# Performance work log

Measured on AMD Instinct MI355X. Metric: run time of the kernel, lower is better.

Reference implementation:

```python
import jax, jax.numpy as jnp
import numpy as np

N = 50000          # nodes
E = 1_600_000      # edges (avg degree 32)
FEAT = 128         # nfeat == nhid
HID = 128
L = 3              # nconvs
C = 10             # nclass
G = 128            # graphs in batch
BN_EPS = 1e-5


def setup_inputs() -> dict:
    key = jax.random.key(0)
    ks = jax.random.split(key, 8)
    x = jax.random.normal(ks[0], (N, FEAT), dtype=jnp.float32)
    edge_index = jax.random.randint(ks[1], (2, E), 0, N, dtype=jnp.int64)
    batch = jnp.sort(jax.random.randint(ks[2], (N,), 0, G, dtype=jnp.int64))
    # stacked per-layer MLP params (nfeat == nhid so shapes are uniform)
    W1 = jax.random.normal(ks[3], (L, FEAT, HID), dtype=jnp.float32) * 0.05
    b1 = jnp.zeros((L, HID), dtype=jnp.float32)
    W2 = jax.random.normal(ks[4], (L, HID, HID), dtype=jnp.float32) * 0.05
    b2 = jnp.zeros((L, HID), dtype=jnp.float32)
    # BatchNorm (eval mode: running stats)
    gamma = jnp.ones((L, HID), dtype=jnp.float32)
    beta = jnp.zeros((L, HID), dtype=jnp.float32)
    rmean = jnp.zeros((L, HID), dtype=jnp.float32)
    rvar = jnp.ones((L, HID), dtype=jnp.float32)
    fc_w = jax.random.normal(ks[5], (HID, C), dtype=jnp.float32) * 0.05
    fc_b = jnp.zeros((C,), dtype=jnp.float32)
    return {
        "x": x, "edge_index": edge_index, "batch": batch,
        "W1": W1, "b1": b1, "W2": W2, "b2": b2,
        "gamma": gamma, "beta": beta, "rmean": rmean, "rvar": rvar,
        "fc_w": fc_w, "fc_b": fc_b,
    }


def reference(x, edge_index, batch, W1, b1, W2, b2, gamma, beta, rmean, rvar, fc_w, fc_b):
    src, dst = edge_index[0], edge_index[1]
    for l in range(L):
        # GINConv aggregation: h_i = (1 + eps) * x_i + sum_{j -> i} x_j  (eps = 0)
        agg = jax.ops.segment_sum(x[src], dst, num_segments=N)  # [N, d] scatter-add
        h = x + agg
        # MLP: Linear -> ReLU -> Linear -> BatchNorm (eval: running stats)
        h = jax.nn.relu(h @ W1[l] + b1[l])
        h = h @ W2[l] + b2[l]
        h = (h - rmean[l]) * jax.lax.rsqrt(rvar[l] + BN_EPS) * gamma[l] + beta[l]
        # outer ReLU; dropout is identity at inference
        x = jax.nn.relu(h)
    # global mean pool over batch ids
    counts = jax.ops.segment_sum(jnp.ones((N,), x.dtype), batch, num_segments=G)
    pooled = jax.ops.segment_sum(x, batch, num_segments=G)
    pooled = pooled / jnp.clip(counts, 1.0)[:, None]  # [G, HID]
    logits = pooled @ fc_w + fc_b                      # [G, C]
    return jax.nn.log_softmax(logits, axis=1)
```

## Files before the change

kernel.cpp:

```cpp
#include <hip/hip_runtime.h>

#define NN 50000
#define EE 1600000
#define GG 128
#define NC 10

#define SB_N   49
#define SB_PAD 36864
#define BK_N   782
#define BK_PAD 2560
#define CHUNK  4096
#define NBLK1  391
#define SLICES 9

typedef __attribute__((ext_vector_type(8))) short bf16x8;
typedef __attribute__((ext_vector_type(4))) float f32x4;
typedef unsigned short u16;

__device__ inline u16 f2bf(float x){
  unsigned u = __builtin_bit_cast(unsigned, x);
  u += 0x7fffu + ((u >> 16) & 1u);
  return (u16)(u >> 16);
}
__device__ inline float bf2f(u16 u){
  return __builtin_bit_cast(float, ((unsigned)u) << 16);
}

__global__ void k_zero_int(int* __restrict__ p, int n){
  int i = blockIdx.x * 256 + threadIdx.x;
  if (i < n) p[i] = 0;
}

__global__ __launch_bounds__(256) void k_scatL1(const int* __restrict__ srcI, const int* __restrict__ dstI,
                                                int* __restrict__ scur, int* __restrict__ sstg){
  __shared__ int hist[SB_N];
  __shared__ int base[64];
  __shared__ int gadj[SB_N];
  __shared__ unsigned reo[CHUNK];
  int t = threadIdx.x;
  int e0 = blockIdx.x * CHUNK;
  int cnt = EE - e0; if (cnt > CHUNK) cnt = CHUNK;
  if (t < SB_N) hist[t] = 0;
  __syncthreads();
  unsigned p[16]; int rk[16];
  #pragma unroll
  for (int r = 0; r < 16; ++r){
    int i = r * 256 + t;
    if (i < cnt){
      unsigned d = (unsigned)dstI[e0 + i];
      p[r] = (d << 16) | (unsigned)srcI[e0 + i];
      rk[r] = atomicAdd(&hist[d >> 10], 1);
    }
  }
  __syncthreads();
  if (t < 64) base[t] = (t < SB_N) ? hist[t] : 0;
  __syncthreads();
  for (int off = 1; off < 64; off <<= 1){
    int a = (t < 64 && t >= off) ? base[t - off] : 0;
    __syncthreads();
    if (t < 64) base[t] += a;
    __syncthreads();
  }
  if (t < SB_N){
    int ex = base[t] - hist[t];
    gadj[t] = atomicAdd(&scur[t], hist[t]) - ex;
  }
  __syncthreads();
  #pragma unroll
  for (int r = 0; r < 16; ++r){
    int i = r * 256 + t;
    if (i < cnt){
      unsigned sb = p[r] >> 26;
      reo[(base[sb] - hist[sb]) + rk[r]] = p[r];
    }
  }
  __syncthreads();
  for (int q = t; q < cnt; q += 256){
    unsigned v = reo[q];
    unsigned sb = v >> 26;
    int off = gadj[sb] + q;
    if ((unsigned)off < SB_PAD) sstg[sb * SB_PAD + off] = (int)v;
  }
}

__global__ __launch_bounds__(256) void k_scatL2(const int* __restrict__ sstg, const int* __restrict__ scur,
                                                int* __restrict__ bcur, int* __restrict__ bstg){
  __shared__ int hist[16];
  __shared__ int base[16];
  __shared__ int gadj[16];
  __shared__ unsigned reo[CHUNK];
  int t = threadIdx.x;
  int sb = blockIdx.x / SLICES;
  int sl = blockIdx.x % SLICES;
  int ssz = scur[sb]; if (ssz > SB_PAD) ssz = SB_PAD;
  int i0 = sl * CHUNK;
  int cnt = ssz - i0;
  if (cnt <= 0) return;
  if (cnt > CHUNK) cnt = CHUNK;
  if (t < 16) hist[t] = 0;
  __syncthreads();
  unsigned p[16]; int rk[16];
  #pragma unroll
  for (int r = 0; r < 16; ++r){
    int i = r * 256 + t;
    if (i < cnt){
      p[r] = (unsigned)sstg[sb * SB_PAD + i0 + i];
      rk[r] = atomicAdd(&hist[(p[r] >> 22) & 15], 1);
    }
  }
  __syncthreads();
  if (t < 16) base[t] = hist[t];
  __syncthreads();
  for (int off = 1; off < 16; off <<= 1){
    int a = (t < 16 && t >= off) ? base[t - off] : 0;
    __syncthreads();
    if (t < 16) base[t] += a;
    __syncthreads();
  }
  if (t < 16){
    int ex = base[t] - hist[t];
    gadj[t] = atomicAdd(&bcur[sb * 16 + t], hist[t]) - ex;
  }
  __syncthreads();
  #pragma unroll
  for (int r = 0; r < 16; ++r){
    int i = r * 256 + t;
    if (i < cnt){
      unsigned b = (p[r] >> 22) & 15;
      reo[(base[b] - hist[b]) + rk[r]] = p[r];
    }
  }
  __syncthreads();
  for (int q = t; q < cnt; q += 256){
    unsigned v = reo[q];
    unsigned b = (v >> 22) & 15;
    int off = gadj[b] + q;
    if ((unsigned)off < BK_PAD) bstg[(sb * 16 + b) * BK_PAD + off] = (int)v;
  }
}

__global__ __launch_bounds__(256) void k_finalize(const int* __restrict__ bstg, const int* __restrict__ bcur,
                                                  u16* __restrict__ adj, int2* __restrict__ ndinfo){
  __shared__ unsigned ebuf[BK_PAD];
  __shared__ int hist[64];
  __shared__ int lrs[64];
  __shared__ int lcur[64];
  int b = blockIdx.x;
  int t = threadIdx.x;
  int bsz = bcur[b]; if (bsz > BK_PAD) bsz = BK_PAD;
  if (t < 64) hist[t] = 0;
  __syncthreads();
  for (int i = t; i < bsz; i += 256){
    unsigned p = (unsigned)bstg[b * BK_PAD + i];
    ebuf[i] = p;
    atomicAdd(&hist[(p >> 16) & 63], 1);
  }
  __syncthreads();
  if (t < 64) lrs[t] = hist[t];
  __syncthreads();
  for (int off = 1; off < 64; off <<= 1){
    int a = (t < 64 && t >= off) ? lrs[t - off] : 0;
    __syncthreads();
    if (t < 64) lrs[t] += a;
    __syncthreads();
  }
  if (t < 64){
    int ex = lrs[t] - hist[t];
    lcur[t] = ex;
    int node = b * 64 + t;
    if (node < NN) ndinfo[node] = make_int2(b * BK_PAD + ex, hist[t]);
  }
  __syncthreads();
  for (int i = t; i < bsz; i += 256){
    unsigned p = ebuf[i];
    int slot = atomicAdd(&lcur[(p >> 16) & 63], 1);
    adj[b * BK_PAD + slot] = (u16)(p & 0xffffu);
  }
}

__global__ void k_prep(const float* __restrict__ x, const float* __restrict__ W1f, const float* __restrict__ W2f,
                       const float* __restrict__ b1, const float* __restrict__ b2,
                       const float* __restrict__ gma, const float* __restrict__ bta,
                       const float* __restrict__ rmn, const float* __restrict__ rvr,
                       u16* __restrict__ xb, u16* __restrict__ Wt,
                       float* __restrict__ SC, float* __restrict__ SH){
  int bid = blockIdx.x;
  int t = threadIdx.x;
  if (bid < 6250){
    int i = bid * 256 + t;
    float4 v = ((const float4*)x)[i];
    ushort4 o;
    o.x = f2bf(v.x); o.y = f2bf(v.y); o.z = f2bf(v.z); o.w = f2bf(v.w);
    ((ushort4*)xb)[i] = o;
  } else if (bid < 6634){
    int i = (bid - 6250) * 256 + t;
    int a = i >> 14; int r = i & 16383; int n = r >> 7; int k = r & 127;
    const float* Wsrc = (a < 3) ? (W1f + a * 16384) : (W2f + (a - 3) * 16384);
    Wt[a * 16384 + n * 128 + k] = f2bf(Wsrc[k * 128 + n]);
  } else {
    for (int i = t; i < 768; i += 256){
      int l = i >> 8; int r = i & 255; int mode = r >> 7; int c = r & 127;
      if (mode == 0){
        SC[(l * 2) * 128 + c] = 1.0f;
        SH[(l * 2) * 128 + c] = b1[l * 128 + c];
      } else {
        float S = gma[l * 128 + c] * rsqrtf(rvr[l * 128 + c] + 1e-5f);
        SC[(l * 2 + 1) * 128 + c] = S;
        SH[(l * 2 + 1) * 128 + c] = (b2[l * 128 + c] - rmn[l * 128 + c]) * S + bta[l * 128 + c];
      }
    }
  }
}

__global__ __launch_bounds__(256) void k_agg(const u16* __restrict__ xb, u16* __restrict__ hb,
                                             const u16* __restrict__ adj,
                                             const int2* __restrict__ ndinfo){
  int t = threadIdx.x;
  int node = blockIdx.x * 16 + (t >> 4);
  int lane = t & 15;
  const bf16x8* xv = (const bf16x8*)xb;
  bf16x8 sv = xv[(long)node * 16 + lane];
  float a[8];
  #pragma unroll
  for (int j = 0; j < 8; ++j) a[j] = bf2f((u16)sv[j]);
  int2 nd = ndinfo[node];
  int r0 = nd.x;
  int d  = nd.y;
  int j = 0;
  for (; j + 8 <= d; j += 8){
    bf16x8 v[8];
    #pragma unroll
    for (int u = 0; u < 8; ++u){
      int s = adj[r0 + j + u];
      v[u] = xv[(long)s * 16 + lane];
    }
    #pragma unroll
    for (int q = 0; q < 8; ++q){
      float s01 = bf2f((u16)v[0][q]) + bf2f((u16)v[1][q]);
      float s23 = bf2f((u16)v[2][q]) + bf2f((u16)v[3][q]);
      float s45 = bf2f((u16)v[4][q]) + bf2f((u16)v[5][q]);
      float s67 = bf2f((u16)v[6][q]) + bf2f((u16)v[7][q]);
      a[q] += (s01 + s23) + (s45 + s67);
    }
  }
  for (; j + 4 <= d; j += 4){
    bf16x8 v0 = xv[(long)adj[r0 + j + 0] * 16 + lane];
    bf16x8 v1 = xv[(long)adj[r0 + j + 1] * 16 + lane];
    bf16x8 v2 = xv[(long)adj[r0 + j + 2] * 16 + lane];
    bf16x8 v3 = xv[(long)adj[r0 + j + 3] * 16 + lane];
    #pragma unroll
    for (int q = 0; q < 8; ++q)
      a[q] += (bf2f((u16)v0[q]) + bf2f((u16)v1[q])) + (bf2f((u16)v2[q]) + bf2f((u16)v3[q]));
  }
  for (; j < d; ++j){
    bf16x8 v0 = xv[(long)adj[r0 + j] * 16 + lane];
    #pragma unroll
    for (int q = 0; q < 8; ++q) a[q] += bf2f((u16)v0[q]);
  }
  bf16x8 o;
  #pragma unroll
  for (int j2 = 0; j2 < 8; ++j2) o[j2] = (short)f2bf(a[j2]);
  ((bf16x8*)hb)[(long)node * 16 + lane] = o;
}

template<int POOL>
__global__ __launch_bounds__(256, 2) void k_mlp(const u16* __restrict__ Ain,
                                                const u16* __restrict__ Wt1,
                                                const u16* __restrict__ Wt2,
                                                const float* __restrict__ B1,
                                                const float* __restrict__ SC2,
                                                const float* __restrict__ SH2,
                                                const int* __restrict__ batch,
                                                u16* __restrict__ Out,
                                                float* __restrict__ pooled){
  __shared__ u16 W2s[16384];
  __shared__ u16 Hs[4][16][128];
  __shared__ float P1[128], P2[128], P3[128];
  int t = threadIdx.x;

  #pragma unroll
  for (int i = 0; i < 8; ++i){
    int c = t + 256 * i;
    int r = c >> 4, cc = c & 15;
    unsigned byte = (unsigned)(r * 256 + cc * 16) ^ (unsigned)((r & 7) << 4);
    *(bf16x8*)((char*)W2s + byte) = *(const bf16x8*)(Wt2 + c * 8);
  }
  if (t < 128){ P1[t] = B1[t]; P2[t] = SC2[t]; P3[t] = SH2[t]; }

  int wv = t >> 6;
  int l  = t & 63;
  int m  = l & 15;
  int kb = l >> 4;

  bf16x8 w1[8][4];
  #pragma unroll
  for (int mt = 0; mt < 8; ++mt)
    #pragma unroll
    for (int ks = 0; ks < 4; ++ks)
      w1[mt][ks] = *(const bf16x8*)(Wt1 + (mt * 16 + m) * 128 + ks * 32 + kb * 8);

  __syncthreads();

  char* hs = (char*)&Hs[wv][0][0];
  unsigned mswz = (unsigned)((m & 7) << 4);
  int gw = blockIdx.x * 4 + wv;
  const int NW = gridDim.x * 4;

  for (int tile = gw; tile < 3125; tile += NW){
    long row0 = (long)tile * 16;
    f32x4 acc[8] = {};
    #pragma unroll
    for (int ks = 0; ks < 4; ++ks){
      bf16x8 h = *(const bf16x8*)(Ain + (row0 + m) * 128 + ks * 32 + kb * 8);
      #pragma unroll
      for (int mt = 0; mt < 8; ++mt)
        acc[mt] = __builtin_amdgcn_mfma_f32_16x16x32_bf16(w1[mt][ks], h, acc[mt], 0, 0, 0);
    }
    #pragma unroll
    for (int mt = 0; mt < 8; ++mt){
      int c0 = mt * 16 + kb * 4;
      float4 bb = *(const float4*)&P1[c0];
      ushort4 o;
      o.x = f2bf(fmaxf(acc[mt][0] + bb.x, 0.f));
      o.y = f2bf(fmaxf(acc[mt][1] + bb.y, 0.f));
      o.z = f2bf(fmaxf(acc[mt][2] + bb.z, 0.f));
      o.w = f2bf(fmaxf(acc[mt][3] + bb.w, 0.f));
      unsigned byte = (unsigned)(m * 256 + c0 * 2) ^ mswz;
      *(ushort4*)(hs + byte) = o;
    }
    f32x4 acc2[8] = {};
    #pragma unroll
    for (int ks = 0; ks < 4; ++ks){
      unsigned hb_ = (unsigned)(m * 256 + ks * 64 + kb * 16) ^ mswz;
      bf16x8 h2 = *(const bf16x8*)(hs + hb_);
      #pragma unroll
      for (int mt = 0; mt < 8; ++mt){
        unsigned wb = (unsigned)((mt * 16 + m) * 256 + ks * 64 + kb * 16) ^ mswz;
        bf16x8 w2 = *(const bf16x8*)((char*)W2s + wb);
        acc2[mt] = __builtin_amdgcn_mfma_f32_16x16x32_bf16(w2, h2, acc2[mt], 0, 0, 0);
      }
    }
    if (!POOL){
      #pragma unroll
      for (int mt = 0; mt < 8; ++mt){
        int c0 = mt * 16 + kb * 4;
        float4 sc = *(const float4*)&P2[c0];
        float4 sh = *(const float4*)&P3[c0];
        ushort4 o;
        o.x = f2bf(fmaxf(acc2[mt][0] * sc.x + sh.x, 0.f));
        o.y = f2bf(fmaxf(acc2[mt][1] * sc.y + sh.y, 0.f));
        o.z = f2bf(fmaxf(acc2[mt][2] * sc.z + sh.z, 0.f));
        o.w = f2bf(fmaxf(acc2[mt][3] * sc.w + sh.w, 0.f));
        *(ushort4*)(Out + (row0 + m) * 128 + c0) = o;
      }
    } else {
      int b0 = batch[row0];
      int b15 = batch[row0 + 15];
      if (b0 == b15){
        #pragma unroll
        for (int mt = 0; mt < 8; ++mt){
          int c0 = mt * 16 + kb * 4;
          float4 sc = *(const float4*)&P2[c0];
          float4 sh = *(const float4*)&P3[c0];
          float v0 = fmaxf(acc2[mt][0] * sc.x + sh.x, 0.f);
          float v1 = fmaxf(acc2[mt][1] * sc.y + sh.y, 0.f);
          float v2 = fmaxf(acc2[mt][2] * sc.z + sh.z, 0.f);
          float v3 = fmaxf(acc2[mt][3] * sc.w + sh.w, 0.f);
          #pragma unroll
          for (int off = 1; off < 16; off <<= 1){
            v0 += __shfl_xor(v0, off);
            v1 += __shfl_xor(v1, off);
            v2 += __shfl_xor(v2, off);
            v3 += __shfl_xor(v3, off);
          }
          if (m == 0){
            float* pg = pooled + b0 * 128 + c0;
            atomicAdd(pg + 0, v0); atomicAdd(pg + 1, v1);
            atomicAdd(pg + 2, v2); atomicAdd(pg + 3, v3);
          }
        }
      } else {
        int bm = batch[row0 + m];
        #pragma unroll
        for (int mt = 0; mt < 8; ++mt){
          int c0 = mt * 16 + kb * 4;
          float4 sc = *(const float4*)&P2[c0];
          float4 sh = *(const float4*)&P3[c0];
          float* pg = pooled + bm * 128 + c0;
          atomicAdd(pg + 0, fmaxf(acc2[mt][0] * sc.x + sh.x, 0.f));
          atomicAdd(pg + 1, fmaxf(acc2[mt][1] * sc.y + sh.y, 0.f));
          atomicAdd(pg + 2, fmaxf(acc2[mt][2] * sc.z + sh.z, 0.f));
          atomicAdd(pg + 3, fmaxf(acc2[mt][3] * sc.w + sh.w, 0.f));
        }
      }
    }
  }
}

__global__ void k_head(const float* __restrict__ pooled, const float* __restrict__ fcw,
                       const float* __restrict__ fcb, const int* __restrict__ batch,
                       float* __restrict__ out){
  int g = threadIdx.x;
  int lo, hi;
  { int a = 0, b = NN; while (a < b){ int mm = (a + b) >> 1; if (batch[mm] < g) a = mm + 1; else b = mm; } lo = a; }
  { int a = lo, b = NN; while (a < b){ int mm = (a + b) >> 1; if (batch[mm] < g + 1) a = mm + 1; else b = mm; } hi = a; }
  float inv = 1.0f / fmaxf((float)(hi - lo), 1.0f);
  float logit[NC];
  #pragma unroll
  for (int c = 0; c < NC; ++c) logit[c] = fcb[c];
  for (int k = 0; k < 128; ++k){
    float pv = pooled[g * 128 + k] * inv;
    #pragma unroll
    for (int c = 0; c < NC; ++c) logit[c] += pv * fcw[k * NC + c];
  }
  float m = logit[0];
  #pragma unroll
  for (int c = 1; c < NC; ++c) m = fmaxf(m, logit[c]);
  float sum = 0.f;
  #pragma unroll
  for (int c = 0; c < NC; ++c) sum += expf(logit[c] - m);
  float ls = logf(sum);
  #pragma unroll
  for (int c = 0; c < NC; ++c) out[g * NC + c] = logit[c] - m - ls;
}

extern "C" void kernel_launch(void* const* d_in, const int* in_sizes, int n_in,
                              void* d_out, int out_size, void* d_ws, size_t ws_size,
                              hipStream_t stream) {
  const float* x     = (const float*)d_in[0];
  const int*   eidx  = (const int*)  d_in[1];
  const int*   batch = (const int*)  d_in[2];
  const float* W1    = (const float*)d_in[3];
  const float* b1    = (const float*)d_in[4];
  const float* W2    = (const float*)d_in[5];
  const float* b2    = (const float*)d_in[6];
  const float* gma   = (const float*)d_in[7];
  const float* bta   = (const float*)d_in[8];
  const float* rmn   = (const float*)d_in[9];
  const float* rvr   = (const float*)d_in[10];
  const float* fcw   = (const float*)d_in[11];
  const float* fcb   = (const float*)d_in[12];
  float* out = (float*)d_out;

  const int* srcI = eidx;
  const int* dstI = eidx + EE;

  u16* bufX = (u16*)d_ws;
  u16* bufA = bufX + 6400000;
  u16* bufB = bufA + 6400000;
  u16* Wt   = bufB + 6400000;
  float* SC = (float*)(Wt + 98304);
  float* SH = SC + 768;
  float* pooled = SH + 768;
  int* ctr  = (int*)(pooled + 16384);
  int* scur = ctr;
  int* bcur = ctr + 64;
  u16* adj  = (u16*)(ctr + 848);
  int2* ndinfo = (int2*)(adj + (BK_N * BK_PAD));
  int* sstg = (int*)bufA;
  int* bstg = (int*)bufB;

  k_zero_int<<<68, 256, 0, stream>>>((int*)pooled, 16384 + 848);

  k_scatL1  <<<NBLK1, 256, 0, stream>>>(srcI, dstI, scur, sstg);
  k_scatL2  <<<SB_N * SLICES, 256, 0, stream>>>(sstg, scur, bcur, bstg);
  k_finalize<<<BK_N, 256, 0, stream>>>(bstg, bcur, adj, ndinfo);

  k_prep<<<6635, 256, 0, stream>>>(x, W1, W2, b1, b2, gma, bta, rmn, rvr, bufX, Wt, SC, SH);

  k_agg   <<<3125, 256, 0, stream>>>(bufX, bufA, adj, ndinfo);
  k_mlp<0><<<391, 256, 0, stream>>>(bufA, Wt + 0 * 16384, Wt + 3 * 16384,
                                    SH + 0 * 128, SC + 1 * 128, SH + 1 * 128, batch, bufB, pooled);
  k_agg   <<<3125, 256, 0, stream>>>(bufB, bufA, adj, ndinfo);
  k_mlp<0><<<391, 256, 0, stream>>>(bufA, Wt + 1 * 16384, Wt + 4 * 16384,
                                    SH + 2 * 128, SC + 3 * 128, SH + 3 * 128, batch, bufB, pooled);
  k_agg   <<<3125, 256, 0, stream>>>(bufB, bufA, adj, ndinfo);
  k_mlp<1><<<391, 256, 0, stream>>>(bufA, Wt + 2 * 16384, Wt + 5 * 16384,
                                    SH + 4 * 128, SC + 5 * 128, SH + 5 * 128, batch, bufB, pooled);

  k_head<<<1, 128, 0, stream>>>(pooled, fcw, fcb, batch, out);
}
```

Measured before the change: 473.0 us.

## Split MLP output columns across waves, keep both weight slices in registers

The fused MLP kernel now has the four waves of a block share one 16-row tile, with each wave computing 32 of the 128 output columns. The first layer's output goes through double-buffered shared memory with a block barrier. Both W1 and W2 slices live in registers, which removes the 32KB shared W2 copy and its per-tile LDS reads, and the grid grows from 391 to 1024 blocks with a higher occupancy hint. In exchange it adds a __syncthreads per tile, each wave re-reads the same input rows, and each wave issues fewer MFMAs per load.

```diff
diff --git a/kernel.cpp b/kernel.cpp
--- a/kernel.cpp
+++ b/kernel.cpp
@@ -264,7 +264,7 @@
 }
 
 template<int POOL>
-__global__ __launch_bounds__(256, 2) void k_mlp(const u16* __restrict__ Ain,
+__global__ __launch_bounds__(256, 4) void k_mlp(const u16* __restrict__ Ain,
                                                 const u16* __restrict__ Wt1,
                                                 const u16* __restrict__ Wt2,
                                                 const float* __restrict__ B1,
@@ -273,84 +273,71 @@
                                                 const int* __restrict__ batch,
                                                 u16* __restrict__ Out,
                                                 float* __restrict__ pooled){
-  __shared__ u16 W2s[16384];
-  __shared__ u16 Hs[4][16][128];
+  __shared__ u16 Hs[2][16][128];
   __shared__ float P1[128], P2[128], P3[128];
   int t = threadIdx.x;
-
-  #pragma unroll
-  for (int i = 0; i < 8; ++i){
-    int c = t + 256 * i;
-    int r = c >> 4, cc = c & 15;
-    unsigned byte = (unsigned)(r * 256 + cc * 16) ^ (unsigned)((r & 7) << 4);
-    *(bf16x8*)((char*)W2s + byte) = *(const bf16x8*)(Wt2 + c * 8);
-  }
   if (t < 128){ P1[t] = B1[t]; P2[t] = SC2[t]; P3[t] = SH2[t]; }
 
   int wv = t >> 6;
   int l  = t & 63;
   int m  = l & 15;
   int kb = l >> 4;
-
-  bf16x8 w1[8][4];
-  #pragma unroll
-  for (int mt = 0; mt < 8; ++mt)
-    #pragma unroll
-    for (int ks = 0; ks < 4; ++ks)
-      w1[mt][ks] = *(const bf16x8*)(Wt1 + (mt * 16 + m) * 128 + ks * 32 + kb * 8);
-
-  __syncthreads();
-
-  char* hs = (char*)&Hs[wv][0][0];
+  int mt0 = wv * 2;
+
+  bf16x8 w1[2][4], w2[2][4];
+  #pragma unroll
+  for (int mtl = 0; mtl < 2; ++mtl)
+    #pragma unroll
+    for (int ks = 0; ks < 4; ++ks){
+      w1[mtl][ks] = *(const bf16x8*)(Wt1 + ((mt0 + mtl) * 16 + m) * 128 + ks * 32 + kb * 8);
+      w2[mtl][ks] = *(const bf16x8*)(Wt2 + ((mt0 + mtl) * 16 + m) * 128 + ks * 32 + kb * 8);
+    }
+  __syncthreads();
+
   unsigned mswz = (unsigned)((m & 7) << 4);
-  int gw = blockIdx.x * 4 + wv;
-  const int NW = gridDim.x * 4;
-
-  for (int tile = gw; tile < 3125; tile += NW){
+
+  for (int tile = blockIdx.x; tile < 3125; tile += gridDim.x){
     long row0 = (long)tile * 16;
-    f32x4 acc[8] = {};
+    char* hs = (char*)&Hs[tile & 1][0][0];
+    f32x4 acc0 = {}, acc1 = {};
     #pragma unroll
     for (int ks = 0; ks < 4; ++ks){
       bf16x8 h = *(const bf16x8*)(Ain + (row0 + m) * 128 + ks * 32 + kb * 8);
-      #pragma unroll
-      for (int mt = 0; mt < 8; ++mt)
-        acc[mt] = __builtin_amdgcn_mfma_f32_16x16x32_bf16(w1[mt][ks], h, acc[mt], 0, 0, 0);
-    }
-    #pragma unroll
-    for (int mt = 0; mt < 8; ++mt){
-      int c0 = mt * 16 + kb * 4;
+      acc0 = __builtin_amdgcn_mfma_f32_16x16x32_bf16(w1[0][ks], h, acc0, 0, 0, 0);
+      acc1 = __builtin_amdgcn_mfma_f32_16x16x32_bf16(w1[1][ks], h, acc1, 0, 0, 0);
+    }
+    #pragma unroll
+    for (int mtl = 0; mtl < 2; ++mtl){
+      const f32x4& av = mtl ? acc1 : acc0;
+      int c0 = (mt0 + mtl) * 16 + kb * 4;
       float4 bb = *(const float4*)&P1[c0];
       ushort4 o;
-      o.x = f2bf(fmaxf(acc[mt][0] + bb.x, 0.f));
-      o.y = f2bf(fmaxf(acc[mt][1] + bb.y, 0.f));
-      o.z = f2bf(fmaxf(acc[mt][2] + bb.z, 0.f));
-      o.w = f2bf(fmaxf(acc[mt][3] + bb.w, 0.f));
-      unsigned byte = (unsigned)(m * 256 + c0 * 2) ^ mswz;
-      *(ushort4*)(hs + byte) = o;
-    }
-    f32x4 acc2[8] = {};
+      o.x = f2bf(fmaxf(av[0] + bb.x, 0.f));
+      o.y = f2bf(fmaxf(av[1] + bb.y, 0.f));
+      o.z = f2bf(fmaxf(av[2] + bb.z, 0.f));
+      o.w = f2bf(fmaxf(av[3] + bb.w, 0.f));
+      *(ushort4*)(hs + ((unsigned)(m * 256 + c0 * 2) ^ mswz)) = o;
+    }
+    __syncthreads();
+    f32x4 acc2_0 = {}, acc2_1 = {};
     #pragma unroll
     for (int ks = 0; ks < 4; ++ks){
-      unsigned hb_ = (unsigned)(m * 256 + ks * 64 + kb * 16) ^ mswz;
-      bf16x8 h2 = *(const bf16x8*)(hs + hb_);
-      #pragma unroll
-      for (int mt = 0; mt < 8; ++mt){
-        unsigned wb = (unsigned)((mt * 16 + m) * 256 + ks * 64 + kb * 16) ^ mswz;
-        bf16x8 w2 = *(const bf16x8*)((char*)W2s + wb);
-        acc2[mt] = __builtin_amdgcn_mfma_f32_16x16x32_bf16(w2, h2, acc2[mt], 0, 0, 0);
-      }
+      bf16x8 h2 = *(const bf16x8*)(hs + ((unsigned)(m * 256 + ks * 64 + kb * 16) ^ mswz));
+      acc2_0 = __builtin_amdgcn_mfma_f32_16x16x32_bf16(w2[0][ks], h2, acc2_0, 0, 0, 0);
+      acc2_1 = __builtin_amdgcn_mfma_f32_16x16x32_bf16(w2[1][ks], h2, acc2_1, 0, 0, 0);
     }
     if (!POOL){
       #pragma unroll
-      for (int mt = 0; mt < 8; ++mt){
-        int c0 = mt * 16 + kb * 4;
+      for (int mtl = 0; mtl < 2; ++mtl){
+        const f32x4& av = mtl ? acc2_1 : acc2_0;
+        int c0 = (mt0 + mtl) * 16 + kb * 4;
         float4 sc = *(const float4*)&P2[c0];
         float4 sh = *(const float4*)&P3[c0];
         ushort4 o;
-        o.x = f2bf(fmaxf(acc2[mt][0] * sc.x + sh.x, 0.f));
-        o.y = f2bf(fmaxf(acc2[mt][1] * sc.y + sh.y, 0.f));
-        o.z = f2bf(fmaxf(acc2[mt][2] * sc.z + sh.z, 0.f));
-        o.w = f2bf(fmaxf(acc2[mt][3] * sc.w + sh.w, 0.f));
+        o.x = f2bf(fmaxf(av[0] * sc.x + sh.x, 0.f));
+        o.y = f2bf(fmaxf(av[1] * sc.y + sh.y, 0.f));
+        o.z = f2bf(fmaxf(av[2] * sc.z + sh.z, 0.f));
+        o.w = f2bf(fmaxf(av[3] * sc.w + sh.w, 0.f));
         *(ushort4*)(Out + (row0 + m) * 128 + c0) = o;
       }
     } else {
@@ -358,14 +345,15 @@
       int b15 = batch[row0 + 15];
       if (b0 == b15){
         #pragma unroll
-        for (int mt = 0; mt < 8; ++mt){
-          int c0 = mt * 16 + kb * 4;
+        for (int mtl = 0; mtl < 2; ++mtl){
+          const f32x4& av = mtl ? acc2_1 : acc2_0;
+          int c0 = (mt0 + mtl) * 16 + kb * 4;
           float4 sc = *(const float4*)&P2[c0];
           float4 sh = *(const float4*)&P3[c0];
-          float v0 = fmaxf(acc2[mt][0] * sc.x + sh.x, 0.f);
-          float v1 = fmaxf(acc2[mt][1] * sc.y + sh.y, 0.f);
-          float v2 = fmaxf(acc2[mt][2] * sc.z + sh.z, 0.f);
-          float v3 = fmaxf(acc2[mt][3] * sc.w + sh.w, 0.f);
+          float v0 = fmaxf(av[0] * sc.x + sh.x, 0.f);
+          float v1 = fmaxf(av[1] * sc.y + sh.y, 0.f);
+          float v2 = fmaxf(av[2] * sc.z + sh.z, 0.f);
+          float v3 = fmaxf(av[3] * sc.w + sh.w, 0.f);
           #pragma unroll
           for (int off = 1; off < 16; off <<= 1){
             v0 += __shfl_xor(v0, off);
@@ -382,15 +370,16 @@
       } else {
         int bm = batch[row0 + m];
         #pragma unroll
-        for (int mt = 0; mt < 8; ++mt){
-          int c0 = mt * 16 + kb * 4;
+        for (int mtl = 0; mtl < 2; ++mtl){
+          const f32x4& av = mtl ? acc2_1 : acc2_0;
+          int c0 = (mt0 + mtl) * 16 + kb * 4;
           float4 sc = *(const float4*)&P2[c0];
           float4 sh = *(const float4*)&P3[c0];
           float* pg = pooled + bm * 128 + c0;
-          atomicAdd(pg + 0, fmaxf(acc2[mt][0] * sc.x + sh.x, 0.f));
-          atomicAdd(pg + 1, fmaxf(acc2[mt][1] * sc.y + sh.y, 0.f));
-          atomicAdd(pg + 2, fmaxf(acc2[mt][2] * sc.z + sh.z, 0.f));
-          atomicAdd(pg + 3, fmaxf(acc2[mt][3] * sc.w + sh.w, 0.f));
+          atomicAdd(pg + 0, fmaxf(av[0] * sc.x + sh.x, 0.f));
+          atomicAdd(pg + 1, fmaxf(av[1] * sc.y + sh.y, 0.f));
+          atomicAdd(pg + 2, fmaxf(av[2] * sc.z + sh.z, 0.f));
+          atomicAdd(pg + 3, fmaxf(av[3] * sc.w + sh.w, 0.f));
         }
       }
     }
@@ -469,14 +458,14 @@
   k_prep<<<6635, 256, 0, stream>>>(x, W1, W2, b1, b2, gma, bta, rmn, rvr, bufX, Wt, SC, SH);
 
   k_agg   <<<3125, 256, 0, stream>>>(bufX, bufA, adj, ndinfo);
-  k_mlp<0><<<391, 256, 0, stream>>>(bufA, Wt + 0 * 16384, Wt + 3 * 16384,
-                                    SH + 0 * 128, SC + 1 * 128, SH + 1 * 128, batch, bufB, pooled);
+  k_mlp<0><<<1024, 256, 0, stream>>>(bufA, Wt + 0 * 16384, Wt + 3 * 16384,
+                                     SH + 0 * 128, SC + 1 * 128, SH + 1 * 128, batch, bufB, pooled);
   k_agg   <<<3125, 256, 0, stream>>>(bufB, bufA, adj, ndinfo);
-  k_mlp<0><<<391, 256, 0, stream>>>(bufA, Wt + 1 * 16384, Wt + 4 * 16384,
-                                    SH + 2 * 128, SC + 3 * 128, SH + 3 * 128, batch, bufB, pooled);
+  k_mlp<0><<<1024, 256, 0, stream>>>(bufA, Wt + 1 * 16384, Wt + 4 * 16384,
+                                     SH + 2 * 128, SC + 3 * 128, SH + 3 * 128, batch, bufB, pooled);
   k_agg   <<<3125, 256, 0, stream>>>(bufB, bufA, adj, ndinfo);
-  k_mlp<1><<<391, 256, 0, stream>>>(bufA, Wt + 2 * 16384, Wt + 5 * 16384,
-                                    SH + 4 * 128, SC + 5 * 128, SH + 5 * 128, batch, bufB, pooled);
+  k_mlp<1><<<1024, 256, 0, stream>>>(bufA, Wt + 2 * 16384, Wt + 5 * 16384,
+                                     SH + 4 * 128, SC + 5 * 128, SH + 5 * 128, batch, bufB, pooled);
 
   k_head<<<1, 128, 0, stream>>>(pooled, fcw, fcb, batch, out);
 }
```

Result: faster. 400.3 us (-15.4%).

## Stage both MLP weight matrices in LDS and prefetch next tile's activations

Applied to the files above, without the earlier changes.

The first-layer weights move out of the per-thread register array (128 VGPRs of fragments) into swizzled shared memory alongside W2. This frees registers, and the freed space is used to software-prefetch the next tile's input rows while the current tile's second GEMM and epilogue run. Bias and BN scale/shift are now read straight from global memory instead of LDS, and the grid grows from 391 to 512 blocks. The trade is more LDS traffic (64KB of weights per block, which may limit occupancy) in exchange for lower register pressure and better overlap of memory latency.

```diff
diff --git a/kernel.cpp b/kernel.cpp
--- a/kernel.cpp
+++ b/kernel.cpp
@@ -273,79 +273,90 @@
                                                 const int* __restrict__ batch,
                                                 u16* __restrict__ Out,
                                                 float* __restrict__ pooled){
-  __shared__ u16 W2s[16384];
-  __shared__ u16 Hs[4][16][128];
-  __shared__ float P1[128], P2[128], P3[128];
-  int t = threadIdx.x;
-
-  #pragma unroll
-  for (int i = 0; i < 8; ++i){
-    int c = t + 256 * i;
-    int r = c >> 4, cc = c & 15;
-    unsigned byte = (unsigned)(r * 256 + cc * 16) ^ (unsigned)((r & 7) << 4);
-    *(bf16x8*)((char*)W2s + byte) = *(const bf16x8*)(Wt2 + c * 8);
-  }
-  if (t < 128){ P1[t] = B1[t]; P2[t] = SC2[t]; P3[t] = SH2[t]; }
+  __shared__ u16 Wl[2][16384];
+  __shared__ u16 Hb[4][2048];
+  int t = threadIdx.x;
+
+  #pragma unroll
+  for (int w = 0; w < 2; ++w){
+    const u16* src = w ? Wt2 : Wt1;
+    #pragma unroll
+    for (int i = 0; i < 8; ++i){
+      int c = t + 256 * i;
+      int r = c >> 4, cc = c & 15;
+      unsigned byte = (unsigned)(r * 256 + cc * 16) ^ (unsigned)((r & 7) << 4);
+      *(bf16x8*)((char*)Wl[w] + byte) = *(const bf16x8*)(src + c * 8);
+    }
+  }
+  __syncthreads();
 
   int wv = t >> 6;
   int l  = t & 63;
   int m  = l & 15;
   int kb = l >> 4;
-
-  bf16x8 w1[8][4];
-  #pragma unroll
-  for (int mt = 0; mt < 8; ++mt)
-    #pragma unroll
-    for (int ks = 0; ks < 4; ++ks)
-      w1[mt][ks] = *(const bf16x8*)(Wt1 + (mt * 16 + m) * 128 + ks * 32 + kb * 8);
-
-  __syncthreads();
-
-  char* hs = (char*)&Hs[wv][0][0];
+  char* hb  = (char*)Hb[wv];
+  char* w1p = (char*)Wl[0];
+  char* w2p = (char*)Wl[1];
   unsigned mswz = (unsigned)((m & 7) << 4);
-  int gw = blockIdx.x * 4 + wv;
+
+  int tile = blockIdx.x * 4 + wv;
   const int NW = gridDim.x * 4;
-
-  for (int tile = gw; tile < 3125; tile += NW){
+  bf16x8 h[4];
+  if (tile < 3125){
+    long r = (long)tile * 16 + m;
+    #pragma unroll
+    for (int ks = 0; ks < 4; ++ks) h[ks] = *(const bf16x8*)(Ain + r * 128 + ks * 32 + kb * 8);
+  }
+
+  while (tile < 3125){
     long row0 = (long)tile * 16;
     f32x4 acc[8] = {};
     #pragma unroll
-    for (int ks = 0; ks < 4; ++ks){
-      bf16x8 h = *(const bf16x8*)(Ain + (row0 + m) * 128 + ks * 32 + kb * 8);
+    for (int mt = 0; mt < 8; ++mt){
+      unsigned rb = (unsigned)((mt * 16 + m) * 256) ^ mswz;
       #pragma unroll
-      for (int mt = 0; mt < 8; ++mt)
-        acc[mt] = __builtin_amdgcn_mfma_f32_16x16x32_bf16(w1[mt][ks], h, acc[mt], 0, 0, 0);
+      for (int ks = 0; ks < 4; ++ks){
+        bf16x8 wf = *(const bf16x8*)(w1p + (rb ^ (unsigned)(ks * 64 + kb * 16)));
+        acc[mt] = __builtin_amdgcn_mfma_f32_16x16x32_bf16(wf, h[ks], acc[mt], 0, 0, 0);
+      }
+    }
+    int ntile = tile + NW;
+    if (ntile < 3125){
+      long r = (long)ntile * 16 + m;
+      #pragma unroll
+      for (int ks = 0; ks < 4; ++ks) h[ks] = *(const bf16x8*)(Ain + r * 128 + ks * 32 + kb * 8);
     }
     #pragma unroll
     for (int mt = 0; mt < 8; ++mt){
       int c0 = mt * 16 + kb * 4;
-      float4 bb = *(const float4*)&P1[c0];
+      float4 bb = *(const float4*)(B1 + c0);
       ushort4 o;
       o.x = f2bf(fmaxf(acc[mt][0] + bb.x, 0.f));
       o.y = f2bf(fmaxf(acc[mt][1] + bb.y, 0.f));
       o.z = f2bf(fmaxf(acc[mt][2] + bb.z, 0.f));
       o.w = f2bf(fmaxf(acc[mt][3] + bb.w, 0.f));
-      unsigned byte = (unsigned)(m * 256 + c0 * 2) ^ mswz;
-      *(ushort4*)(hs + byte) = o;
-    }
+      *(ushort4*)(hb + ((unsigned)(m * 256 + c0 * 2) ^ mswz)) = o;
+    }
+    bf16x8 h2[4];
+    #pragma unroll
+    for (int ks = 0; ks < 4; ++ks)
+      h2[ks] = *(const bf16x8*)(hb + ((unsigned)(m * 256 + ks * 64 + kb * 16) ^ mswz));
     f32x4 acc2[8] = {};
     #pragma unroll
-    for (int ks = 0; ks < 4; ++ks){
-      unsigned hb_ = (unsigned)(m * 256 + ks * 64 + kb * 16) ^ mswz;
-      bf16x8 h2 = *(const bf16x8*)(hs + hb_);
+    for (int mt = 0; mt < 8; ++mt){
+      unsigned rb = (unsigned)((mt * 16 + m) * 256) ^ mswz;
       #pragma unroll
-      for (int mt = 0; mt < 8; ++mt){
-        unsigned wb = (unsigned)((mt * 16 + m) * 256 + ks * 64 + kb * 16) ^ mswz;
-        bf16x8 w2 = *(const bf16x8*)((char*)W2s + wb);
-        acc2[mt] = __builtin_amdgcn_mfma_f32_16x16x32_bf16(w2, h2, acc2[mt], 0, 0, 0);
+      for (int ks = 0; ks < 4; ++ks){
+        bf16x8 wf = *(const bf16x8*)(w2p + (rb ^ (unsigned)(ks * 64 + kb * 16)));
+        acc2[mt] = __builtin_amdgcn_mfma_f32_16x16x32_bf16(wf, h2[ks], acc2[mt], 0, 0, 0);
       }
     }
     if (!POOL){
       #pragma unroll
       for (int mt = 0; mt < 8; ++mt){
         int c0 = mt * 16 + kb * 4;
-        float4 sc = *(const float4*)&P2[c0];
-        float4 sh = *(const float4*)&P3[c0];
+        float4 sc = *(const float4*)(SC2 + c0);
+        float4 sh = *(const float4*)(SH2 + c0);
         ushort4 o;
         o.x = f2bf(fmaxf(acc2[mt][0] * sc.x + sh.x, 0.f));
         o.y = f2bf(fmaxf(acc2[mt][1] * sc.y + sh.y, 0.f));
@@ -360,8 +371,8 @@
         #pragma unroll
         for (int mt = 0; mt < 8; ++mt){
           int c0 = mt * 16 + kb * 4;
-          float4 sc = *(const float4*)&P2[c0];
-          float4 sh = *(const float4*)&P3[c0];
+          float4 sc = *(const float4*)(SC2 + c0);
+          float4 sh = *(const float4*)(SH2 + c0);
           float v0 = fmaxf(acc2[mt][0] * sc.x + sh.x, 0.f);
           float v1 = fmaxf(acc2[mt][1] * sc.y + sh.y, 0.f);
           float v2 = fmaxf(acc2[mt][2] * sc.z + sh.z, 0.f);
@@ -384,8 +395,8 @@
         #pragma unroll
         for (int mt = 0; mt < 8; ++mt){
           int c0 = mt * 16 + kb * 4;
-          float4 sc = *(const float4*)&P2[c0];
-          float4 sh = *(const float4*)&P3[c0];
+          float4 sc = *(const float4*)(SC2 + c0);
+          float4 sh = *(const float4*)(SH2 + c0);
           float* pg = pooled + bm * 128 + c0;
           atomicAdd(pg + 0, fmaxf(acc2[mt][0] * sc.x + sh.x, 0.f));
           atomicAdd(pg + 1, fmaxf(acc2[mt][1] * sc.y + sh.y, 0.f));
@@ -394,6 +405,7 @@
         }
       }
     }
+    tile = ntile;
   }
 }
 
@@ -469,13 +481,13 @@
   k_prep<<<6635, 256, 0, stream>>>(x, W1, W2, b1, b2, gma, bta, rmn, rvr, bufX, Wt, SC, SH);
 
   k_agg   <<<3125, 256, 0, stream>>>(bufX, bufA, adj, ndinfo);
-  k_mlp<0><<<391, 256, 0, stream>>>(bufA, Wt + 0 * 16384, Wt + 3 * 16384,
+  k_mlp<0><<<512, 256, 0, stream>>>(bufA, Wt + 0 * 16384, Wt + 3 * 16384,
                                     SH + 0 * 128, SC + 1 * 128, SH + 1 * 128, batch, bufB, pooled);
   k_agg   <<<3125, 256, 0, stream>>>(bufB, bufA, adj, ndinfo);
-  k_mlp<0><<<391, 256, 0, stream>>>(bufA, Wt + 1 * 16384, Wt + 4 * 16384,
+  k_mlp<0><<<512, 256, 0, stream>>>(bufA, Wt + 1 * 16384, Wt + 4 * 16384,
                                     SH + 2 * 128, SC + 3 * 128, SH + 3 * 128, batch, bufB, pooled);
   k_agg   <<<3125, 256, 0, stream>>>(bufB, bufA, adj, ndinfo);
-  k_mlp<1><<<391, 256, 0, stream>>>(bufA, Wt + 2 * 16384, Wt + 5 * 16384,
+  k_mlp<1><<<512, 256, 0, stream>>>(bufA, Wt + 2 * 16384, Wt + 5 * 16384,
                                     SH + 4 * 128, SC + 5 * 128, SH + 5 * 128, batch, bufB, pooled);
 
   k_head<<<1, 128, 0, stream>>>(pooled, fcw, fcb, batch, out);
```

Result: slower. 498.2 us (+5.3%).

## Split fused two-layer MLP kernel into separate single-GEMM launches

Applied to the files above, without the earlier changes.

The fused MLP kernel, which kept the intermediate activation in LDS and staged W2 in shared memory, is replaced by a generic single-GEMM kernel launched twice per layer. Each GEMM keeps its weights in registers and applies a per-channel scale/shift plus ReLU read directly from global memory. This removes the LDS staging, the intermediate-activation round-trips through LDS and the block barrier. In exchange, each layer now writes and re-reads the 50000x128 bf16 intermediate through global memory and pays an extra launch. It also relies on the first layer's SC being set up as 1 so it reproduces the bias-only epilogue.

```diff
diff --git a/kernel.cpp b/kernel.cpp
--- a/kernel.cpp
+++ b/kernel.cpp
@@ -264,47 +264,25 @@
 }
 
 template<int POOL>
-__global__ __launch_bounds__(256, 2) void k_mlp(const u16* __restrict__ Ain,
-                                                const u16* __restrict__ Wt1,
-                                                const u16* __restrict__ Wt2,
-                                                const float* __restrict__ B1,
-                                                const float* __restrict__ SC2,
-                                                const float* __restrict__ SH2,
-                                                const int* __restrict__ batch,
-                                                u16* __restrict__ Out,
-                                                float* __restrict__ pooled){
-  __shared__ u16 W2s[16384];
-  __shared__ u16 Hs[4][16][128];
-  __shared__ float P1[128], P2[128], P3[128];
-  int t = threadIdx.x;
-
-  #pragma unroll
-  for (int i = 0; i < 8; ++i){
-    int c = t + 256 * i;
-    int r = c >> 4, cc = c & 15;
-    unsigned byte = (unsigned)(r * 256 + cc * 16) ^ (unsigned)((r & 7) << 4);
-    *(bf16x8*)((char*)W2s + byte) = *(const bf16x8*)(Wt2 + c * 8);
-  }
-  if (t < 128){ P1[t] = B1[t]; P2[t] = SC2[t]; P3[t] = SH2[t]; }
-
-  int wv = t >> 6;
-  int l  = t & 63;
+__global__ __launch_bounds__(256, 2) void k_gemm(const u16* __restrict__ Ain,
+                                                 const u16* __restrict__ Wt,
+                                                 const float* __restrict__ SC,
+                                                 const float* __restrict__ SH,
+                                                 const int* __restrict__ batch,
+                                                 u16* __restrict__ Out,
+                                                 float* __restrict__ pooled){
+  int gw = (blockIdx.x * 256 + threadIdx.x) >> 6;
+  int l  = threadIdx.x & 63;
   int m  = l & 15;
   int kb = l >> 4;
-
-  bf16x8 w1[8][4];
+  const int NW = (gridDim.x * 256) >> 6;
+
+  bf16x8 w[8][4];
   #pragma unroll
   for (int mt = 0; mt < 8; ++mt)
     #pragma unroll
     for (int ks = 0; ks < 4; ++ks)
-      w1[mt][ks] = *(const bf16x8*)(Wt1 + (mt * 16 + m) * 128 + ks * 32 + kb * 8);
-
-  __syncthreads();
-
-  char* hs = (char*)&Hs[wv][0][0];
-  unsigned mswz = (unsigned)((m & 7) << 4);
-  int gw = blockIdx.x * 4 + wv;
-  const int NW = gridDim.x * 4;
+      w[mt][ks] = *(const bf16x8*)(Wt + (mt * 16 + m) * 128 + ks * 32 + kb * 8);
 
   for (int tile = gw; tile < 3125; tile += NW){
     long row0 = (long)tile * 16;
@@ -314,43 +292,20 @@
       bf16x8 h = *(const bf16x8*)(Ain + (row0 + m) * 128 + ks * 32 + kb * 8);
       #pragma unroll
       for (int mt = 0; mt < 8; ++mt)
-        acc[mt] = __builtin_amdgcn_mfma_f32_16x16x32_bf16(w1[mt][ks], h, acc[mt], 0, 0, 0);
-    }
-    #pragma unroll
-    for (int mt = 0; mt < 8; ++mt){
-      int c0 = mt * 16 + kb * 4;
-      float4 bb = *(const float4*)&P1[c0];
-      ushort4 o;
-      o.x = f2bf(fmaxf(acc[mt][0] + bb.x, 0.f));
-      o.y = f2bf(fmaxf(acc[mt][1] + bb.y, 0.f));
-      o.z = f2bf(fmaxf(acc[mt][2] + bb.z, 0.f));
-      o.w = f2bf(fmaxf(acc[mt][3] + bb.w, 0.f));
-      unsigned byte = (unsigned)(m * 256 + c0 * 2) ^ mswz;
-      *(ushort4*)(hs + byte) = o;
-    }
-    f32x4 acc2[8] = {};
-    #pragma unroll
-    for (int ks = 0; ks < 4; ++ks){
-      unsigned hb_ = (unsigned)(m * 256 + ks * 64 + kb * 16) ^ mswz;
-      bf16x8 h2 = *(const bf16x8*)(hs + hb_);
-      #pragma unroll
-      for (int mt = 0; mt < 8; ++mt){
-        unsigned wb = (unsigned)((mt * 16 + m) * 256 + ks * 64 + kb * 16) ^ mswz;
-        bf16x8 w2 = *(const bf16x8*)((char*)W2s + wb);
-        acc2[mt] = __builtin_amdgcn_mfma_f32_16x16x32_bf16(w2, h2, acc2[mt], 0, 0, 0);
-      }
+        acc[mt] = __builtin_amdgcn_mfma_f32_16x16x32_bf16(w[mt][ks], h, acc[mt], 0, 0, 0);
     }
     if (!POOL){
       #pragma unroll
       for (int mt = 0; mt < 8; ++mt){
         int c0 = mt * 16 + kb * 4;
-        float4 sc = *(const float4*)&P2[c0];
-        float4 sh = *(const float4*)&P3[c0];
+        float4 sc = *(const float4*)(SC + c0);
+        float4 sh = *(const float4*)(SH + c0);
+        float v0 = fmaxf(acc[mt][0] * sc.x + sh.x, 0.f);
+        float v1 = fmaxf(acc[mt][1] * sc.y + sh.y, 0.f);
+        float v2 = fmaxf(acc[mt][2] * sc.z + sh.z, 0.f);
+        float v3 = fmaxf(acc[mt][3] * sc.w + sh.w, 0.f);
         ushort4 o;
-        o.x = f2bf(fmaxf(acc2[mt][0] * sc.x + sh.x, 0.f));
-        o.y = f2bf(fmaxf(acc2[mt][1] * sc.y + sh.y, 0.f));
-        o.z = f2bf(fmaxf(acc2[mt][2] * sc.z + sh.z, 0.f));
-        o.w = f2bf(fmaxf(acc2[mt][3] * sc.w + sh.w, 0.f));
+        o.x = f2bf(v0); o.y = f2bf(v1); o.z = f2bf(v2); o.w = f2bf(v3);
         *(ushort4*)(Out + (row0 + m) * 128 + c0) = o;
       }
     } else {
@@ -360,12 +315,12 @@
         #pragma unroll
         for (int mt = 0; mt < 8; ++mt){
           int c0 = mt * 16 + kb * 4;
-          float4 sc = *(const float4*)&P2[c0];
-          float4 sh = *(const float4*)&P3[c0];
-          float v0 = fmaxf(acc2[mt][0] * sc.x + sh.x, 0.f);
-          float v1 = fmaxf(acc2[mt][1] * sc.y + sh.y, 0.f);
-          float v2 = fmaxf(acc2[mt][2] * sc.z + sh.z, 0.f);
-          float v3 = fmaxf(acc2[mt][3] * sc.w + sh.w, 0.f);
+          float4 sc = *(const float4*)(SC + c0);
+          float4 sh = *(const float4*)(SH + c0);
+          float v0 = fmaxf(acc[mt][0] * sc.x + sh.x, 0.f);
+          float v1 = fmaxf(acc[mt][1] * sc.y + sh.y, 0.f);
+          float v2 = fmaxf(acc[mt][2] * sc.z + sh.z, 0.f);
+          float v3 = fmaxf(acc[mt][3] * sc.w + sh.w, 0.f);
           #pragma unroll
           for (int off = 1; off < 16; off <<= 1){
             v0 += __shfl_xor(v0, off);
@@ -384,13 +339,13 @@
         #pragma unroll
         for (int mt = 0; mt < 8; ++mt){
           int c0 = mt * 16 + kb * 4;
-          float4 sc = *(const float4*)&P2[c0];
-          float4 sh = *(const float4*)&P3[c0];
+          float4 sc = *(const float4*)(SC + c0);
+          float4 sh = *(const float4*)(SH + c0);
           float* pg = pooled + bm * 128 + c0;
-          atomicAdd(pg + 0, fmaxf(acc2[mt][0] * sc.x + sh.x, 0.f));
-          atomicAdd(pg + 1, fmaxf(acc2[mt][1] * sc.y + sh.y, 0.f));
-          atomicAdd(pg + 2, fmaxf(acc2[mt][2] * sc.z + sh.z, 0.f));
-          atomicAdd(pg + 3, fmaxf(acc2[mt][3] * sc.w + sh.w, 0.f));
+          atomicAdd(pg + 0, fmaxf(acc[mt][0] * sc.x + sh.x, 0.f));
+          atomicAdd(pg + 1, fmaxf(acc[mt][1] * sc.y + sh.y, 0.f));
+          atomicAdd(pg + 2, fmaxf(acc[mt][2] * sc.z + sh.z, 0.f));
+          atomicAdd(pg + 3, fmaxf(acc[mt][3] * sc.w + sh.w, 0.f));
         }
       }
     }
@@ -468,15 +423,15 @@
 
   k_prep<<<6635, 256, 0, stream>>>(x, W1, W2, b1, b2, gma, bta, rmn, rvr, bufX, Wt, SC, SH);
 
-  k_agg   <<<3125, 256, 0, stream>>>(bufX, bufA, adj, ndinfo);
-  k_mlp<0><<<391, 256, 0, stream>>>(bufA, Wt + 0 * 16384, Wt + 3 * 16384,
-                                    SH + 0 * 128, SC + 1 * 128, SH + 1 * 128, batch, bufB, pooled);
-  k_agg   <<<3125, 256, 0, stream>>>(bufB, bufA, adj, ndinfo);
-  k_mlp<0><<<391, 256, 0, stream>>>(bufA, Wt + 1 * 16384, Wt + 4 * 16384,
-                                    SH + 2 * 128, SC + 3 * 128, SH + 3 * 128, batch, bufB, pooled);
-  k_agg   <<<3125, 256, 0, stream>>>(bufB, bufA, adj, ndinfo);
-  k_mlp<1><<<391, 256, 0, stream>>>(bufA, Wt + 2 * 16384, Wt + 5 * 16384,
-                                    SH + 4 * 128, SC + 5 * 128, SH + 5 * 128, batch, bufB, pooled);
+  k_agg    <<<3125, 256, 0, stream>>>(bufX, bufA, adj, ndinfo);
+  k_gemm<0><<<256, 256, 0, stream>>>(bufA, Wt + 0 * 16384, SC + 0 * 128, SH + 0 * 128, batch, bufB, pooled);
+  k_gemm<0><<<256, 256, 0, stream>>>(bufB, Wt + 3 * 16384, SC + 1 * 128, SH + 1 * 128, batch, bufA, pooled);
+  k_agg    <<<3125, 256, 0, stream>>>(bufA, bufB, adj, ndinfo);
+  k_gemm<0><<<256, 256, 0, stream>>>(bufB, Wt + 1 * 16384, SC + 2 * 128, SH + 2 * 128, batch, bufX, pooled);
+  k_gemm<0><<<256, 256, 0, stream>>>(bufX, Wt + 4 * 16384, SC + 3 * 128, SH + 3 * 128, batch, bufB, pooled);
+  k_agg    <<<3125, 256, 0, stream>>>(bufB, bufA, adj, ndinfo);
+  k_gemm<0><<<256, 256, 0, stream>>>(bufA, Wt + 2 * 16384, SC + 4 * 128, SH + 4 * 128, batch, bufX, pooled);
+  k_gemm<1><<<256, 256, 0, stream>>>(bufX, Wt + 5 * 16384, SC + 5 * 128, SH + 5 * 128, batch, bufA, pooled);
 
   k_head<<<1, 128, 0, stream>>>(pooled, fcw, fcb, batch, out);
 }
```

Measured after the change: 435.4 us. 8.0% less time.
